# Optimization experiments

Measured on AMD Instinct MI355X. Metric: run time of the kernel, lower is better.

Reference implementation:

```python
import jax, jax.numpy as jnp
import numpy as np

N_CLASS = 8
N_CH = 32
H = 256
W = 256
BATCH = 8


def setup_inputs() -> dict:
    key = jax.random.key(0)
    k1, k2, k3 = jax.random.split(key, 3)
    x = jax.random.normal(k1, (BATCH, H, W, N_CH), dtype=jnp.float32)
    # keras 'uniform' initializer ~ U(-0.05, 0.05); add identity to scale so the
    # lower-triangular factor is well conditioned (setup choice, not math change).
    mean = jax.random.uniform(k2, (N_CLASS, N_CH), jnp.float32, -0.05, 0.05)
    scale = jax.random.uniform(k3, (N_CLASS, N_CH, N_CH), jnp.float32, -0.05, 0.05)
    scale = scale + jnp.eye(N_CH, dtype=jnp.float32)
    return {"x": x, "mean": mean, "scale": scale}


def reference(x, mean, scale):
    # x: [B,H,W,C]; mean: [K,C]; scale: [K,C,C] (lower-tri factor per class)
    B = x.shape[0]
    xf = x.reshape(B, H * W, N_CH)                    # [B,N,C]
    L = jnp.tril(scale)                               # tfd MVNTriL uses lower triangle
    eye = jnp.eye(N_CH, dtype=L.dtype)
    Linv = jax.vmap(lambda l: jax.scipy.linalg.solve_triangular(l, eye, lower=True))(L)  # [K,C,C]
    diff = xf[:, :, None, :] - mean[None, None, :, :]  # [B,N,K,C]
    z = jnp.einsum('kcd,bnkd->bnkc', Linv, diff)       # whitened residual
    maha = jnp.sum(z * z, axis=-1)                     # [B,N,K]
    log_det = jnp.sum(jnp.log(jnp.abs(jnp.diagonal(L, axis1=-2, axis2=-1))), axis=-1)  # [K]
    LOG_2PI = jnp.log(jnp.asarray(2.0 * np.pi, dtype=x.dtype))
    log_prob = -0.5 * maha - 0.5 * N_CH * LOG_2PI - log_det[None, None, :]
    prob = jnp.exp(log_prob)                           # [B,N,K] mvn.prob(x) per class
    # tf.nn.l2_normalize over class axis: x * rsqrt(max(sum(x^2), eps))
    g = prob * jax.lax.rsqrt(jnp.maximum(jnp.sum(prob * prob, axis=-1, keepdims=True), 1e-12))
    # output[..., i*C + j] = gauss[..., i] * x[..., j]
    out = (g[:, :, :, None] * xf[:, :, None, :]).reshape(B, H, W, N_CLASS * N_CH)
    return out
```

## Files before the change

### kernel.cpp

```cpp
#include <hip/hip_runtime.h>
#include <math.h>

#define NCH   32
#define NCLS  8
#define NPIX  (8 * 256 * 256)
#define TRI   528

__device__ float g_tri[NCLS * TRI];
__device__ float g_offn[NCLS * NCH];
__device__ float g_lc2[NCLS];

__global__ __launch_bounds__(256) void setup_kernel(const float* __restrict__ mean,
                                                    const float* __restrict__ scale) {
  __shared__ float sinv[NCLS][NCH][NCH];
  const int t = threadIdx.x;
  const int k = t >> 5;
  const int j = t & 31;
  const float* L = scale + k * NCH * NCH;

  double y[NCH];
  #pragma unroll
  for (int i = 0; i < NCH; ++i) {
    double s = (i == j) ? 1.0 : 0.0;
    #pragma unroll
    for (int m = 0; m < i; ++m) s -= (double)L[i * NCH + m] * y[m];
    y[i] = (i < j) ? 0.0 : (s / (double)L[i * NCH + i]);
  }
  #pragma unroll
  for (int i = 0; i < NCH; ++i) sinv[k][i][j] = (float)y[i];
  __syncthreads();

  {
    const int base = k * TRI + j * (j + 1) / 2;
    for (int m = 0; m <= j; ++m) g_tri[base + m] = sinv[k][j][m];
  }
  {
    double o = 0.0;
    for (int m = 0; m <= j; ++m) o += (double)sinv[k][j][m] * (double)mean[k * NCH + m];
    g_offn[k * NCH + j] = (float)(-o);
  }
  if (j == 0) {
    double ld = 0.0;
    for (int i = 0; i < NCH; ++i) ld += log(fabs((double)L[i * NCH + i]));
    const double LOG_2PI = 1.8378770664093454836;
    const double LOG2E   = 1.4426950408889634074;
    g_lc2[k] = (float)((-0.5 * NCH * LOG_2PI - ld) * LOG2E);
  }
}

__global__ __launch_bounds__(256, 3) void fuzzy_main(const float* __restrict__ x,
                                                     float* __restrict__ out) {
  __shared__ float xs[256 * NCH];
  __shared__ float gs[256 * 9];
  const int t = threadIdx.x;
  const long long pixBase = (long long)blockIdx.x * 256;

  {
    const float4* gx = reinterpret_cast<const float4*>(x + pixBase * NCH);
    #pragma unroll
    for (int i = 0; i < 8; ++i) {
      const float4 v = gx[i * 256 + t];
      const int p = i * 32 + (t >> 3);
      const int c = t & 7;
      reinterpret_cast<float4*>(xs)[p * 8 + (c ^ (p & 7))] = v;
    }
  }
  __syncthreads();

  float xv[NCH];
  {
    const float4* row = reinterpret_cast<const float4*>(xs + t * NCH);
    #pragma unroll
    for (int i = 0; i < 8; ++i) {
      const float4 v = row[i ^ (t & 7)];
      xv[4 * i + 0] = v.x; xv[4 * i + 1] = v.y;
      xv[4 * i + 2] = v.z; xv[4 * i + 3] = v.w;
    }
  }

  float s2 = 0.0f;
  #pragma unroll 1
  for (int k = 0; k < NCLS; ++k) {
    const float* __restrict__ tri  = g_tri  + k * TRI;
    const float* __restrict__ offn = g_offn + k * NCH;
    float maha = 0.0f;
    int idx = 0;
    #pragma unroll
    for (int c = 0; c < NCH; ++c) {
      float z = offn[c];
      #pragma unroll
      for (int m = 0; m <= c; ++m) z = fmaf(tri[idx + m], xv[m], z);
      idx += c + 1;
      maha = fmaf(z, z, maha);
    }
    const float p = exp2f(fmaf(maha, -0.72134752044448170368f, g_lc2[k]));
    gs[t * 9 + k] = p;
    s2 = fmaf(p, p, s2);
  }
  gs[t * 9 + 8] = rsqrtf(fmaxf(s2, 1e-12f));
  __syncthreads();

  const int lane = t & 63;
  const int w    = t >> 6;
  const int kk   = lane >> 3;
  const int ch   = lane & 7;
  float* ob = out + (pixBase + (long long)w * 64) * (NCLS * NCH) + lane * 4;
  #pragma unroll 4
  for (int i = 0; i < 64; ++i) {
    const int p = w * 64 + i;
    const float g = gs[p * 9 + kk] * gs[p * 9 + 8];
    const float4 xc = reinterpret_cast<const float4*>(xs)[p * 8 + (ch ^ (p & 7))];
    float4 o;
    o.x = g * xc.x; o.y = g * xc.y; o.z = g * xc.z; o.w = g * xc.w;
    *reinterpret_cast<float4*>(ob) = o;
    ob += NCLS * NCH;
  }
}

extern "C" void kernel_launch(void* const* d_in, const int* in_sizes, int n_in,
                              void* d_out, int out_size, void* d_ws, size_t ws_size,
                              hipStream_t stream) {
  const float* x     = (const float*)d_in[0];
  const float* mean  = (const float*)d_in[1];
  const float* scale = (const float*)d_in[2];
  float* out = (float*)d_out;

  hipLaunchKernelGGL(setup_kernel, dim3(1), dim3(256), 0, stream, mean, scale);
  hipLaunchKernelGGL(fuzzy_main, dim3(NPIX / 256), dim3(256), 0, stream, x, out);
}
```

Baseline: 667.8 us.

## Split fused kernel into gauss computation and separate output expansion kernel

The single fused kernel is split in two. The first computes the normalized per-class gaussian weights and writes them to a global buffer of 8 floats per pixel. The second re-reads x and those weights to write the 256-channel output with a pure streaming store kernel. The aim is to decouple the compute-heavy phase from the store-bound phase so each can use the GPU well on its own, at the cost of reading x a second time plus an extra global write and read of the gauss buffer.

Result: slower. 823.6 us (+23.3%).

```diff
diff --git a/kernel.cpp b/kernel.cpp
--- a/kernel.cpp
+++ b/kernel.cpp
@@ -9,6 +9,7 @@
 __device__ float g_tri[NCLS * TRI];
 __device__ float g_offn[NCLS * NCH];
 __device__ float g_lc2[NCLS];
+__device__ float g_gauss[(size_t)NPIX * NCLS];
 
 __global__ __launch_bounds__(256) void setup_kernel(const float* __restrict__ mean,
                                                     const float* __restrict__ scale) {
@@ -48,8 +49,7 @@
   }
 }
 
-__global__ __launch_bounds__(256, 3) void fuzzy_main(const float* __restrict__ x,
-                                                     float* __restrict__ out) {
+__global__ __launch_bounds__(256, 3) void gauss_kernel(const float* __restrict__ x) {
   __shared__ float xs[256 * NCH];
   __shared__ float gs[256 * 9];
   const int t = threadIdx.x;
@@ -97,23 +97,36 @@
     gs[t * 9 + k] = p;
     s2 = fmaf(p, p, s2);
   }
-  gs[t * 9 + 8] = rsqrtf(fmaxf(s2, 1e-12f));
-  __syncthreads();
+  const float rinv = rsqrtf(fmaxf(s2, 1e-12f));
 
-  const int lane = t & 63;
-  const int w    = t >> 6;
+  float4 a, b;
+  a.x = gs[t * 9 + 0] * rinv; a.y = gs[t * 9 + 1] * rinv;
+  a.z = gs[t * 9 + 2] * rinv; a.w = gs[t * 9 + 3] * rinv;
+  b.x = gs[t * 9 + 4] * rinv; b.y = gs[t * 9 + 5] * rinv;
+  b.z = gs[t * 9 + 6] * rinv; b.w = gs[t * 9 + 7] * rinv;
+  float4* gp = reinterpret_cast<float4*>(g_gauss + (pixBase + t) * NCLS);
+  gp[0] = a; gp[1] = b;
+}
+
+__global__ __launch_bounds__(256) void expand_kernel(const float* __restrict__ x,
+                                                     float* __restrict__ out) {
+  const int wid  = (blockIdx.x << 2) | (threadIdx.x >> 6);
+  const int lane = threadIdx.x & 63;
   const int kk   = lane >> 3;
   const int ch   = lane & 7;
-  float* ob = out + (pixBase + (long long)w * 64) * (NCLS * NCH) + lane * 4;
+  const long long p0 = (long long)wid * 64;
+
+  const float4* __restrict__ x4 = reinterpret_cast<const float4*>(x) + p0 * 8 + ch;
+  const float*  __restrict__ gp = g_gauss + p0 * NCLS + kk;
+  float* __restrict__ op = out + p0 * (NCLS * NCH) + (lane << 2);
+
   #pragma unroll 4
   for (int i = 0; i < 64; ++i) {
-    const int p = w * 64 + i;
-    const float g = gs[p * 9 + kk] * gs[p * 9 + 8];
-    const float4 xc = reinterpret_cast<const float4*>(xs)[p * 8 + (ch ^ (p & 7))];
+    const float4 xc = x4[i * 8];
+    const float  gv = gp[i * 8];
     float4 o;
-    o.x = g * xc.x; o.y = g * xc.y; o.z = g * xc.z; o.w = g * xc.w;
-    *reinterpret_cast<float4*>(ob) = o;
-    ob += NCLS * NCH;
+    o.x = gv * xc.x; o.y = gv * xc.y; o.z = gv * xc.z; o.w = gv * xc.w;
+    *reinterpret_cast<float4*>(op + (long long)i * (NCLS * NCH)) = o;
   }
 }
 
@@ -126,5 +139,6 @@
   float* out = (float*)d_out;
 
   hipLaunchKernelGGL(setup_kernel, dim3(1), dim3(256), 0, stream, mean, scale);
-  hipLaunchKernelGGL(fuzzy_main, dim3(NPIX / 256), dim3(256), 0, stream, x, out);
+  hipLaunchKernelGGL(gauss_kernel, dim3(NPIX / 256), dim3(256), 0, stream, x);
+  hipLaunchKernelGGL(expand_kernel, dim3(NPIX / 256), dim3(256), 0, stream, x, out);
 }
```

## Register-block four pixels per thread and cache whitening factors in LDS

Applied to the files above, without the earlier changes.

Each thread now processes four pixels, so every triangular coefficient read is reused across four FMA chains. The triangular factors, offsets and log constants are staged once per block in shared memory instead of being read from global memory. The block-wide output barrier is replaced by per-wave slabs that are synchronised only with waitcnt. The trade-off is four times fewer blocks, higher register pressure with launch bounds dropped to 2, and less latency hiding for the large output write stream.

Result: slower. 736.2 us (+10.2%).

```diff
diff --git a/kernel.cpp b/kernel.cpp
--- a/kernel.cpp
+++ b/kernel.cpp
@@ -48,72 +48,112 @@
   }
 }
 
-__global__ __launch_bounds__(256, 3) void fuzzy_main(const float* __restrict__ x,
+__global__ __launch_bounds__(256, 2) void fuzzy_main(const float* __restrict__ x,
                                                      float* __restrict__ out) {
-  __shared__ float xs[256 * NCH];
-  __shared__ float gs[256 * 9];
+  __shared__ float  ctri[NCLS * TRI];
+  __shared__ float  coffn[NCLS * NCH];
+  __shared__ float  clc2[NCLS];
+  __shared__ float  gsw[4][256 * 9];
+  __shared__ float4 xslab[4][32 * 8];
+
   const int t = threadIdx.x;
-  const long long pixBase = (long long)blockIdx.x * 256;
+  const int w = t >> 6;
+  const int l = t & 63;
 
+  for (int i = t; i < NCLS * TRI; i += 256) ctri[i] = g_tri[i];
+  if (t < NCLS * NCH) coffn[t] = g_offn[t];
+  if (t < NCLS)       clc2[t]  = g_lc2[t];
+
+  const long long pixW = (long long)blockIdx.x * 1024 + (long long)w * 256;
+  float xv[4][NCH];
   {
-    const float4* gx = reinterpret_cast<const float4*>(x + pixBase * NCH);
+    const float4* __restrict__ x4 = reinterpret_cast<const float4*>(x) + pixW * 8;
     #pragma unroll
-    for (int i = 0; i < 8; ++i) {
-      const float4 v = gx[i * 256 + t];
-      const int p = i * 32 + (t >> 3);
-      const int c = t & 7;
-      reinterpret_cast<float4*>(xs)[p * 8 + (c ^ (p & 7))] = v;
+    for (int j = 0; j < 4; ++j) {
+      #pragma unroll
+      for (int c = 0; c < 8; ++c) {
+        const float4 v = x4[(j * 64 + l) * 8 + c];
+        xv[j][c * 4 + 0] = v.x; xv[j][c * 4 + 1] = v.y;
+        xv[j][c * 4 + 2] = v.z; xv[j][c * 4 + 3] = v.w;
+      }
     }
   }
   __syncthreads();
 
-  float xv[NCH];
-  {
-    const float4* row = reinterpret_cast<const float4*>(xs + t * NCH);
-    #pragma unroll
-    for (int i = 0; i < 8; ++i) {
-      const float4 v = row[i ^ (t & 7)];
-      xv[4 * i + 0] = v.x; xv[4 * i + 1] = v.y;
-      xv[4 * i + 2] = v.z; xv[4 * i + 3] = v.w;
-    }
-  }
-
-  float s2 = 0.0f;
+  float* __restrict__ gslab = gsw[w];
+  float s2_0 = 0.f, s2_1 = 0.f, s2_2 = 0.f, s2_3 = 0.f;
   #pragma unroll 1
   for (int k = 0; k < NCLS; ++k) {
-    const float* __restrict__ tri  = g_tri  + k * TRI;
-    const float* __restrict__ offn = g_offn + k * NCH;
-    float maha = 0.0f;
+    const float* __restrict__ tri = ctri  + k * TRI;
+    const float* __restrict__ off = coffn + k * NCH;
+    const float lk = clc2[k];
+    float mh0 = 0.f, mh1 = 0.f, mh2 = 0.f, mh3 = 0.f;
     int idx = 0;
     #pragma unroll
     for (int c = 0; c < NCH; ++c) {
-      float z = offn[c];
+      const float o = off[c];
+      float z0 = o, z1 = o, z2 = o, z3 = o;
       #pragma unroll
-      for (int m = 0; m <= c; ++m) z = fmaf(tri[idx + m], xv[m], z);
+      for (int m = 0; m <= c; ++m) {
+        const float a = tri[idx + m];
+        z0 = fmaf(a, xv[0][m], z0);
+        z1 = fmaf(a, xv[1][m], z1);
+        z2 = fmaf(a, xv[2][m], z2);
+        z3 = fmaf(a, xv[3][m], z3);
+      }
       idx += c + 1;
-      maha = fmaf(z, z, maha);
+      mh0 = fmaf(z0, z0, mh0); mh1 = fmaf(z1, z1, mh1);
+      mh2 = fmaf(z2, z2, mh2); mh3 = fmaf(z3, z3, mh3);
     }
-    const float p = exp2f(fmaf(maha, -0.72134752044448170368f, g_lc2[k]));
-    gs[t * 9 + k] = p;
-    s2 = fmaf(p, p, s2);
+    const float CEXP = -0.72134752044448170368f;
+    const float p0 = exp2f(fmaf(mh0, CEXP, lk));
+    const float p1 = exp2f(fmaf(mh1, CEXP, lk));
+    const float p2 = exp2f(fmaf(mh2, CEXP, lk));
+    const float p3 = exp2f(fmaf(mh3, CEXP, lk));
+    gslab[(0 * 64 + l) * 9 + k] = p0;
+    gslab[(1 * 64 + l) * 9 + k] = p1;
+    gslab[(2 * 64 + l) * 9 + k] = p2;
+    gslab[(3 * 64 + l) * 9 + k] = p3;
+    s2_0 = fmaf(p0, p0, s2_0); s2_1 = fmaf(p1, p1, s2_1);
+    s2_2 = fmaf(p2, p2, s2_2); s2_3 = fmaf(p3, p3, s2_3);
   }
-  gs[t * 9 + 8] = rsqrtf(fmaxf(s2, 1e-12f));
-  __syncthreads();
+  gslab[(0 * 64 + l) * 9 + 8] = rsqrtf(fmaxf(s2_0, 1e-12f));
+  gslab[(1 * 64 + l) * 9 + 8] = rsqrtf(fmaxf(s2_1, 1e-12f));
+  gslab[(2 * 64 + l) * 9 + 8] = rsqrtf(fmaxf(s2_2, 1e-12f));
+  gslab[(3 * 64 + l) * 9 + 8] = rsqrtf(fmaxf(s2_3, 1e-12f));
 
-  const int lane = t & 63;
-  const int w    = t >> 6;
-  const int kk   = lane >> 3;
-  const int ch   = lane & 7;
-  float* ob = out + (pixBase + (long long)w * 64) * (NCLS * NCH) + lane * 4;
-  #pragma unroll 4
-  for (int i = 0; i < 64; ++i) {
-    const int p = w * 64 + i;
-    const float g = gs[p * 9 + kk] * gs[p * 9 + 8];
-    const float4 xc = reinterpret_cast<const float4*>(xs)[p * 8 + (ch ^ (p & 7))];
-    float4 o;
-    o.x = g * xc.x; o.y = g * xc.y; o.z = g * xc.z; o.w = g * xc.w;
-    *reinterpret_cast<float4*>(ob) = o;
-    ob += NCLS * NCH;
+  float4* __restrict__ xsl = xslab[w];
+  const int ch = l & 7;
+  const int kk = l >> 3;
+  #pragma unroll
+  for (int j = 0; j < 4; ++j) {
+    #pragma unroll
+    for (int half = 0; half < 2; ++half) {
+      if ((l >> 5) == half) {
+        const int r = l & 31;
+        #pragma unroll
+        for (int c = 0; c < 8; ++c) {
+          float4 v;
+          v.x = xv[j][c * 4 + 0]; v.y = xv[j][c * 4 + 1];
+          v.z = xv[j][c * 4 + 2]; v.w = xv[j][c * 4 + 3];
+          xsl[r * 8 + (c ^ (r & 7))] = v;
+        }
+      }
+      asm volatile("s_waitcnt lgkmcnt(0)" ::: "memory");
+
+      const int pbase = j * 64 + half * 32;
+      float* ob = out + (pixW + pbase) * (NCLS * NCH) + (l << 2);
+      #pragma unroll 4
+      for (int i = 0; i < 32; ++i) {
+        const int pw = pbase + i;
+        const float g = gsw[w][pw * 9 + kk] * gsw[w][pw * 9 + 8];
+        const float4 xc = xsl[i * 8 + (ch ^ (i & 7))];
+        float4 o;
+        o.x = g * xc.x; o.y = g * xc.y; o.z = g * xc.z; o.w = g * xc.w;
+        *reinterpret_cast<float4*>(ob + (long long)i * (NCLS * NCH)) = o;
+      }
+      asm volatile("s_waitcnt lgkmcnt(0)" ::: "memory");
+    }
   }
 }
 
@@ -126,5 +166,5 @@
   float* out = (float*)d_out;
 
   hipLaunchKernelGGL(setup_kernel, dim3(1), dim3(256), 0, stream, mean, scale);
-  hipLaunchKernelGGL(fuzzy_main, dim3(NPIX / 256), dim3(256), 0, stream, x, out);
+  hipLaunchKernelGGL(fuzzy_main, dim3(NPIX / 1024), dim3(256), 0, stream, x, out);
 }
```
